# Kernel tuning notes

Measured on AMD Instinct MI355X. Metric: run time of the kernel, lower is better.

## Reference

```python
import jax, jax.numpy as jnp
from jax import lax
import numpy as np

B = 64
INPUT_DIM = 500000
WIN = 500
N_WIN = INPUT_DIM // WIN  # 1000
HID = 30
ANC = 7
KS = 75
EPS = 1e-5


def setup_inputs() -> dict:
    key = jax.random.key(0)
    ks = jax.random.split(key, 8)
    x = jax.random.uniform(ks[0], (B, INPUT_DIM, 2), dtype=jnp.float32)
    # stacked per-window MLP params (PyTorch Linear default init scale ~ 1/sqrt(fan_in))
    W1 = jax.random.normal(ks[1], (N_WIN, WIN, HID), dtype=jnp.float32) / np.sqrt(WIN)
    b1 = jax.random.normal(ks[2], (N_WIN, HID), dtype=jnp.float32) * 0.01
    W2 = jax.random.normal(ks[3], (N_WIN, HID, ANC), dtype=jnp.float32) / np.sqrt(HID)
    b2 = jax.random.normal(ks[4], (N_WIN, ANC), dtype=jnp.float32) * 0.01
    conv_w = jax.random.normal(ks[5], (ANC, ANC, KS, 2), dtype=jnp.float32) / np.sqrt(ANC * KS * 2)
    conv_b = jax.random.normal(ks[6], (ANC,), dtype=jnp.float32) * 0.01
    return {"x": x, "W1": W1, "b1": b1, "W2": W2, "b2": b2,
            "conv_w": conv_w, "conv_b": conv_b}


def _forward_base(xw, W1, b1, W2, b2):
    h = jnp.einsum('bnwc,nwh->bnhc', xw, W1) + b1[None, :, :, None]
    h = jax.nn.relu(h)
    # BatchNorm1d (training mode, affine=False): batch stats per (window, hidden)
    # and per haplotype channel (the torch module is called once per haplotype).
    mean = jnp.mean(h, axis=0, keepdims=True)
    var = jnp.var(h, axis=0, keepdims=True)  # biased, matches torch BN normalization
    h = (h - mean) * lax.rsqrt(var + EPS)
    o = jnp.einsum('bnhc,nha->bnac', h, W2) + b2[None, :, :, None]  # [B,nW,A,2]
    return jnp.transpose(o, (0, 2, 1, 3))  # [B, A, nW, 2]


def reference(x, W1, b1, W2, b2, conv_w, conv_b):
    x = (x - 0.5) * 2.0
    xw = x[:, :N_WIN * WIN].reshape(B, N_WIN, WIN, 2)
    out_base = _forward_base(xw, W1, b1, W2, b2)  # [B, A, nW, 2]
    # smoother: softmax over ancestry dim, reflect-padded Conv2d
    p = jax.nn.softmax(out_base, axis=1)
    pad_h = KS // 2  # 37
    pp = jnp.pad(p, ((0, 0), (0, 0), (pad_h, pad_h), (1, 1)), mode='reflect')
    out = lax.conv_general_dilated(pp, conv_w, window_strides=(1, 1), padding='VALID',
                                   dimension_numbers=('NCHW', 'OIHW', 'NCHW'))
    out = out + conv_b[None, :, None, None]
    out_smooth = out[:, :, :, 0:2]  # crop to 2 haplotype columns
    return out_base, out_smooth
```

## Files before the change

kernel.cpp:

```cpp
#include <hip/hip_runtime.h>

#define NWIN 1000
#define WIN  500
#define HID  30
#define ANC  7
#define BATCH 64
#define KS   75
#define PADH 37
#define OBASE_ELEMS (BATCH*ANC*NWIN*2)

#define CK   24
#define NCK  21

#define XB(buf,c,p,b) ((buf)*3264 + ((c)*24+(p))*68 + (b))
#define WB(buf,p,j)   (6528 + (buf)*768 + (p)*32 + (j))
#define HS(ph,b,col)  (((ph)*64+(b))*61 + (col))

__device__ __forceinline__ void gload_lds16(const float* g, float* l) {
    __builtin_amdgcn_global_load_lds(
        (const __attribute__((address_space(1))) void*)g,
        (__attribute__((address_space(3))) void*)l, 16, 0, 0);
}

__global__ __launch_bounds__(256) void k1(
        const float* __restrict__ x,
        const float* __restrict__ W1, const float* __restrict__ b1,
        const float* __restrict__ W2, const float* __restrict__ b2,
        float* __restrict__ out_base)
{
    __shared__ float smem[8064];

    const int n    = blockIdx.x;
    const int t    = threadIdx.x;
    const int wid  = __builtin_amdgcn_readfirstlane(t >> 6);
    const int lane = t & 63;
    const int bq   = lane & 15;
    const int jq   = lane >> 4;
    const int b0   = bq * 4;
    const int j0   = jq * 8;

    float acc[4][8][2];
#pragma unroll
    for (int i = 0; i < 4; ++i)
#pragma unroll
        for (int j = 0; j < 8; ++j) { acc[i][j][0] = 0.f; acc[i][j][1] = 0.f; }

    int sb[3], sq[3];
#pragma unroll
    for (int r = 0; r < 3; ++r) {
        const int idx = t + r * 256;
        sb[r] = idx / 12;
        sq[r] = idx % 12;
    }

    const float4* __restrict__ x4 = reinterpret_cast<const float4*>(x);
    float4 xr[3];

    auto issue_x = [&](int ck) {
#pragma unroll
        for (int r = 0; r < 3; ++r) {
            int gq = ck * 12 + sq[r];
            if (gq > 249) gq = 249;
            xr[r] = x4[(size_t)sb[r] * 250000u + (size_t)n * 250u + gq];
        }
    };

    auto commit_x = [&](int buf, int ck) {
#pragma unroll
        for (int r = 0; r < 3; ++r) {
            const int p0 = 2 * sq[r], p1 = p0 + 1;
            const bool ok0 = (ck * CK + p0) < 500;
            const bool ok1 = (ck * CK + p1) < 500;
            const int bb = sb[r];
            smem[XB(buf, 0, p0, bb)] = ok0 ? fmaf(2.f, xr[r].x, -1.f) : 0.f;
            smem[XB(buf, 1, p0, bb)] = ok0 ? fmaf(2.f, xr[r].y, -1.f) : 0.f;
            smem[XB(buf, 0, p1, bb)] = ok1 ? fmaf(2.f, xr[r].z, -1.f) : 0.f;
            smem[XB(buf, 1, p1, bb)] = ok1 ? fmaf(2.f, xr[r].w, -1.f) : 0.f;
        }
    };

    auto issue_w = [&](int ck, int buf) {
        if (t < 192) {
            int gp = ck * CK + (t >> 3);
            if (gp > 499) gp = 499;
            const size_t off = (size_t)n * 15000u + (size_t)gp * 30u
                             + (size_t)(t & 7) * 4u;
            gload_lds16(W1 + off, &smem[WB(buf, 0, 0) + (t & 192) * 4]);
        }
    };

    issue_w(0, 0);
    issue_x(0);
    commit_x(0, 0);
    __syncthreads();

    for (int ck = 0; ck < NCK; ++ck) {
        const int cur = ck & 1, nxt = cur ^ 1;
        const bool pre = (ck < NCK - 1);
        if (pre) {
            issue_w(ck + 1, nxt);
            issue_x(ck + 1);
            __builtin_amdgcn_sched_barrier(0);
        }

        const int pb = wid * 6;
#pragma unroll
        for (int i = 0; i < 6; ++i) {
            const int p = pb + i;
            const float4 xa = *reinterpret_cast<const float4*>(&smem[XB(cur, 0, p, b0)]);
            const float4 xb = *reinterpret_cast<const float4*>(&smem[XB(cur, 1, p, b0)]);
            const float4 w0 = *reinterpret_cast<const float4*>(&smem[WB(cur, p, j0)]);
            const float4 w1 = *reinterpret_cast<const float4*>(&smem[WB(cur, p, j0 + 4)]);
            const float xav[4] = {xa.x, xa.y, xa.z, xa.w};
            const float xbv[4] = {xb.x, xb.y, xb.z, xb.w};
            const float wv[8]  = {w0.x, w0.y, w0.z, w0.w, w1.x, w1.y, w1.z, w1.w};
#pragma unroll
            for (int ii = 0; ii < 4; ++ii)
#pragma unroll
                for (int jj = 0; jj < 8; ++jj) {
                    acc[ii][jj][0] = fmaf(xav[ii], wv[jj], acc[ii][jj][0]);
                    acc[ii][jj][1] = fmaf(xbv[ii], wv[jj], acc[ii][jj][1]);
                }
        }

        if (pre) commit_x(nxt, ck + 1);
        __syncthreads();
    }

    if (wid < 2) {
#pragma unroll
        for (int ii = 0; ii < 4; ++ii)
#pragma unroll
            for (int jj = 0; jj < 8; ++jj) {
                const int j = j0 + jj;
                if (j < 30) {
                    smem[HS(wid, b0 + ii, j)]      = acc[ii][jj][0];
                    smem[HS(wid, b0 + ii, 30 + j)] = acc[ii][jj][1];
                }
            }
    }
    __syncthreads();
    if (wid >= 2) {
#pragma unroll
        for (int ii = 0; ii < 4; ++ii)
#pragma unroll
            for (int jj = 0; jj < 8; ++jj) {
                const int j = j0 + jj;
                if (j < 30) {
                    smem[HS(wid - 2, b0 + ii, j)]      += acc[ii][jj][0];
                    smem[HS(wid - 2, b0 + ii, 30 + j)] += acc[ii][jj][1];
                }
            }
    }
    __syncthreads();

    {
        const int bb = t & 63;
        const int q2 = t >> 6;
        const int ch = q2 >> 1;
        const int jh = (q2 & 1) * 15;
        const float* __restrict__ b1p = b1 + n * HID + jh;
#pragma unroll
        for (int jj = 0; jj < 15; ++jj) {
            const int col = ch * 30 + jh + jj;
            float v = smem[HS(0, bb, col)] + smem[HS(1, bb, col)] + b1p[jj];
            v = fmaxf(v, 0.f);
            float s = v;
#pragma unroll
            for (int off = 32; off > 0; off >>= 1) s += __shfl_xor(s, off);
            const float mean = s * (1.f / 64.f);
            const float d = v - mean;
            float ss = d * d;
#pragma unroll
            for (int off = 32; off > 0; off >>= 1) ss += __shfl_xor(ss, off);
            const float var = ss * (1.f / 64.f);
            const float rn  = rsqrtf(var + 1e-5f);
            smem[HS(0, bb, col)] = d * rn;
        }
    }
    __syncthreads();

    const float* __restrict__ w2p = W2 + (size_t)n * (HID * ANC);
    float2* __restrict__ ob2 = reinterpret_cast<float2*>(out_base);
    for (int idx = t; idx < BATCH * ANC; idx += 256) {
        const int bb = idx / 7, a = idx - bb * 7;
        float o0 = b2[n * ANC + a], o1 = o0;
#pragma unroll
        for (int h = 0; h < HID; ++h) {
            const float wv = w2p[h * ANC + a];
            o0 = fmaf(smem[HS(0, bb, h)],      wv, o0);
            o1 = fmaf(smem[HS(0, bb, 30 + h)], wv, o1);
        }
        ob2[((size_t)bb * ANC + a) * NWIN + n] = make_float2(o0, o1);
    }
}

__global__ __launch_bounds__(256, 2) void k2(
        const float* __restrict__ out_base,
        const float* __restrict__ conv_w, const float* __restrict__ conv_b,
        float* __restrict__ out_smooth)
{
    __shared__ float2 sdl[199 * ANC];
    __shared__ float2 wael[ANC * ANC * KS];

    const int bidx = blockIdx.x;
    const int b  = bidx >> 3;
    const int ht = bidx & 7;
    const int h0 = ht * 125;
    const int t  = threadIdx.x;

    const float2* __restrict__ cw2 = reinterpret_cast<const float2*>(conv_w);
    for (int idx = t; idx < ANC * ANC * KS; idx += 256) {
        const float2 w = cw2[idx];
        wael[idx] = make_float2(w.x + w.y, w.x - w.y);
    }

    if (t < 199) {
        const int hglob = h0 - PADH + t;
        const int hm = hglob < 0 ? -hglob
                     : (hglob >= NWIN ? 2 * NWIN - 2 - hglob : hglob);
        float p[2][ANC];
#pragma unroll
        for (int c = 0; c < 2; ++c) {
            float v[ANC];
            float m = -1e30f;
#pragma unroll
            for (int a = 0; a < ANC; ++a) {
                v[a] = out_base[(((size_t)b * ANC + a) * NWIN + hm) * 2 + c];
                m = fmaxf(m, v[a]);
            }
            float s = 0.f;
#pragma unroll
            for (int a = 0; a < ANC; ++a) { v[a] = __expf(v[a] - m); s += v[a]; }
            const float inv = 1.f / s;
#pragma unroll
            for (int a = 0; a < ANC; ++a) p[c][a] = v[a] * inv;
        }
#pragma unroll
        for (int a = 0; a < ANC; ++a)
            sdl[t * ANC + a] = make_float2(p[0][a] + p[1][a], p[0][a] - p[1][a]);
    }
    __syncthreads();

    for (int idx = t; idx < ANC * 125; idx += 256) {
        const int o  = idx / 125;
        const int hl = idx % 125;
        float sa = 0.f, de = 0.f;
        const float2* __restrict__ wrow = &wael[o * ANC * KS];
#pragma unroll 1
        for (int i = 0; i < ANC; ++i) {
            const float2* __restrict__ sdp = &sdl[hl * ANC + i];
            const float2* __restrict__ wp  = &wrow[i * KS];
#pragma unroll 5
            for (int kh = 0; kh < KS; ++kh) {
                const float2 sd = sdp[kh * ANC];
                const float2 we = wp[kh];
                sa = fmaf(sd.x, we.x, sa);
                de = fmaf(sd.y, we.y, de);
            }
        }
        const float cb = conv_b[o];
        const float o0 = 0.5f * (sa - de) + cb;
        const float o1 = 0.5f * (sa + de) + cb;
        const size_t base = (((size_t)b * ANC + o) * NWIN + (h0 + hl)) * 2;
        out_smooth[base + 0] = o0;
        out_smooth[base + 1] = o1;
    }
}

extern "C" void kernel_launch(void* const* d_in, const int* in_sizes, int n_in,
                              void* d_out, int out_size, void* d_ws, size_t ws_size,
                              hipStream_t stream)
{
    const float* x      = (const float*)d_in[0];
    const float* W1     = (const float*)d_in[1];
    const float* b1     = (const float*)d_in[2];
    const float* W2     = (const float*)d_in[3];
    const float* b2     = (const float*)d_in[4];
    const float* conv_w = (const float*)d_in[5];
    const float* conv_b = (const float*)d_in[6];
    float* out = (float*)d_out;

    k1<<<dim3(NWIN), dim3(256), 0, stream>>>(x, W1, b1, W2, b2, out);
    k2<<<dim3(BATCH * 8), dim3(256), 0, stream>>>(out, conv_w, conv_b,
                                                  out + OBASE_ELEMS);
}
```

Measured before the change: 166.6 us.

## Deepen W1 prefetch to a four-slot LDS ring with distance two

W1 chunks now go into a four-slot LDS ring and are prefetched two chunks ahead. The x tiles keep their two-slot buffer. Each barrier now waits with explicit s_waitcnt counts instead of a full drain of outstanding loads, so W1 global-to-LDS loads can stay in flight across iterations, hiding more global memory latency in the GEMM main loop. The cost is more LDS per block and correctness that depends on hand-set waitcnt ordering. Threads 192-255 now repeat the same W1 loads as threads 0-63, adding redundant load traffic.

```diff
diff --git a/kernel.cpp b/kernel.cpp
--- a/kernel.cpp
+++ b/kernel.cpp
@@ -13,7 +13,7 @@
 #define NCK  21
 
 #define XB(buf,c,p,b) ((buf)*3264 + ((c)*24+(p))*68 + (b))
-#define WB(buf,p,j)   (6528 + (buf)*768 + (p)*32 + (j))
+#define WB4(buf,p,j)  (6528 + (buf)*768 + (p)*32 + (j))
 #define HS(ph,b,col)  (((ph)*64+(b))*61 + (col))
 
 __device__ __forceinline__ void gload_lds16(const float* g, float* l) {
@@ -28,7 +28,7 @@
         const float* __restrict__ W2, const float* __restrict__ b2,
         float* __restrict__ out_base)
 {
-    __shared__ float smem[8064];
+    __shared__ float smem[9600];
 
     const int n    = blockIdx.x;
     const int t    = threadIdx.x;
@@ -80,37 +80,23 @@
     };
 
     auto issue_w = [&](int ck, int buf) {
-        if (t < 192) {
-            int gp = ck * CK + (t >> 3);
-            if (gp > 499) gp = 499;
-            const size_t off = (size_t)n * 15000u + (size_t)gp * 30u
-                             + (size_t)(t & 7) * 4u;
-            gload_lds16(W1 + off, &smem[WB(buf, 0, 0) + (t & 192) * 4]);
-        }
+        const int g = (t < 192) ? t : (t - 192);
+        int gp = ck * CK + (g >> 3);
+        if (gp > 499) gp = 499;
+        const size_t off = (size_t)n * 15000u + (size_t)gp * 30u
+                         + (size_t)(g & 7) * 4u;
+        gload_lds16(W1 + off, &smem[6528 + buf * 768 + (g & 192) * 4]);
     };
 
-    issue_w(0, 0);
-    issue_x(0);
-    commit_x(0, 0);
-    __syncthreads();
-
-    for (int ck = 0; ck < NCK; ++ck) {
-        const int cur = ck & 1, nxt = cur ^ 1;
-        const bool pre = (ck < NCK - 1);
-        if (pre) {
-            issue_w(ck + 1, nxt);
-            issue_x(ck + 1);
-            __builtin_amdgcn_sched_barrier(0);
-        }
-
+    auto compute = [&](int cur, int wc) {
         const int pb = wid * 6;
 #pragma unroll
         for (int i = 0; i < 6; ++i) {
             const int p = pb + i;
             const float4 xa = *reinterpret_cast<const float4*>(&smem[XB(cur, 0, p, b0)]);
             const float4 xb = *reinterpret_cast<const float4*>(&smem[XB(cur, 1, p, b0)]);
-            const float4 w0 = *reinterpret_cast<const float4*>(&smem[WB(cur, p, j0)]);
-            const float4 w1 = *reinterpret_cast<const float4*>(&smem[WB(cur, p, j0 + 4)]);
+            const float4 w0 = *reinterpret_cast<const float4*>(&smem[WB4(wc, p, j0)]);
+            const float4 w1 = *reinterpret_cast<const float4*>(&smem[WB4(wc, p, j0 + 4)]);
             const float xav[4] = {xa.x, xa.y, xa.z, xa.w};
             const float xbv[4] = {xb.x, xb.y, xb.z, xb.w};
             const float wv[8]  = {w0.x, w0.y, w0.z, w0.w, w1.x, w1.y, w1.z, w1.w};
@@ -122,10 +108,38 @@
                     acc[ii][jj][1] = fmaf(xbv[ii], wv[jj], acc[ii][jj][1]);
                 }
         }
-
-        if (pre) commit_x(nxt, ck + 1);
-        __syncthreads();
-    }
+    };
+
+    issue_x(0);
+    issue_w(0, 0);
+    commit_x(0, 0);
+    issue_w(1, 1);
+    asm volatile("s_waitcnt vmcnt(1) lgkmcnt(0)" ::: "memory");
+    __builtin_amdgcn_s_barrier();
+
+    for (int ck = 0; ck < NCK - 2; ++ck) {
+        const int cur = ck & 1;
+        issue_x(ck + 1);
+        issue_w(ck + 2, (ck + 2) & 3);
+        __builtin_amdgcn_sched_barrier(0);
+
+        compute(cur, ck & 3);
+
+        commit_x((ck + 1) & 1, ck + 1);
+        asm volatile("s_waitcnt lgkmcnt(0)" ::: "memory");
+        __builtin_amdgcn_s_barrier();
+    }
+
+    {
+        issue_x(NCK - 1);
+        __builtin_amdgcn_sched_barrier(0);
+        compute((NCK - 2) & 1, (NCK - 2) & 3);
+        commit_x((NCK - 1) & 1, NCK - 1);
+        asm volatile("s_waitcnt lgkmcnt(0)" ::: "memory");
+        __builtin_amdgcn_s_barrier();
+    }
+    compute((NCK - 1) & 1, (NCK - 1) & 3);
+    __syncthreads();
 
     if (wid < 2) {
 #pragma unroll
```

After: 166.1 us. No clear change (-0.3%).
